# Performance work log

Hardware: AMD Instinct MI355X
Metric: run time of the kernel (lower is better)

The kernel has to match this reference:

```python
import jax, jax.numpy as jnp
import numpy as np
import math

B, L, D, H = 2, 2048, 1024, 16
HD = D // H  # head dim = 64


def setup_inputs() -> dict:
    key = jax.random.key(0)
    ks = jax.random.split(key, 5)
    s = 0.02
    return {
        "x": jax.random.normal(ks[0], (B, L, D), dtype=jnp.float32),
        "w_qkv": jax.random.normal(ks[1], (D, 3 * D), dtype=jnp.float32) * s,
        "b_qkv": jnp.zeros((3 * D,), dtype=jnp.float32),
        "w_out": jax.random.normal(ks[2], (D, D), dtype=jnp.float32) * s,
        "b_out": jnp.zeros((D,), dtype=jnp.float32),
    }


def reference(x, w_qkv, b_qkv, w_out, b_out):
    Bc, Lc, Dc = x.shape
    qkv = x @ w_qkv + b_qkv  # [B, L, 3D]
    q, k, v = jnp.split(qkv, 3, axis=-1)
    # [B, H, L, hd]
    q = q.reshape(Bc, Lc, H, HD).transpose(0, 2, 1, 3)
    k = k.reshape(Bc, Lc, H, HD).transpose(0, 2, 1, 3)
    v = v.reshape(Bc, Lc, H, HD).transpose(0, 2, 1, 3)
    scores = jnp.einsum("bhqd,bhkd->bhqk", q, k) / math.sqrt(HD)
    causal = jnp.tril(jnp.ones((Lc, Lc), dtype=bool))
    scores = jnp.where(causal[None, None, :, :], scores, -jnp.inf)
    probs = jax.nn.softmax(scores, axis=-1)
    outs = jnp.einsum("bhqk,bhkd->bhqd", probs, v)  # [B, H, L, hd]
    outs = outs.transpose(0, 2, 1, 3).reshape(Bc, Lc, Dc)
    return outs @ w_out + b_out
```

## Files before the change

### kernel.cpp

```cpp
#include <hip/hip_runtime.h>
#include <hip/hip_bf16.h>


using bf16x8 = __attribute__((ext_vector_type(8))) short;
using f32x4  = __attribute__((ext_vector_type(4))) float;

static __device__ __forceinline__ unsigned short f2b(float f) {
  unsigned u = __builtin_bit_cast(unsigned, f);
  unsigned r = (u + 0x7fffu + ((u >> 16) & 1u)) >> 16;
  return (unsigned short)r;
}

static __device__ __forceinline__ unsigned cvtpk(float lo, float hi) {
  unsigned r;
  asm("v_cvt_pk_bf16_f32 %0, %1, %2" : "=v"(r) : "v"(lo), "v"(hi));
  return r;
}

static __device__ __forceinline__ void gl_lds16(const void* g, void* l) {
  __builtin_amdgcn_global_load_lds(
      (const __attribute__((address_space(1))) unsigned int*)g,
      (__attribute__((address_space(3))) unsigned int*)l, 16, 0, 0);
}

__global__ __launch_bounds__(256) void prep_inputs(
    const float* __restrict__ x, const float* __restrict__ w_qkv,
    const float* __restrict__ w_out, unsigned short* __restrict__ xb,
    unsigned short* __restrict__ wqkvt, unsigned short* __restrict__ woutt) {
  const int bid = blockIdx.x, t = threadIdx.x;
  if (bid < 2048) {
    int i = bid * 256 + t;
    const float4* p = reinterpret_cast<const float4*>(x) + (size_t)i * 2;
    float4 a = p[0], b = p[1];
    bf16x8 o;
    o[0] = f2b(a.x); o[1] = f2b(a.y); o[2] = f2b(a.z); o[3] = f2b(a.w);
    o[4] = f2b(b.x); o[5] = f2b(b.y); o[6] = f2b(b.z); o[7] = f2b(b.w);
    reinterpret_cast<bf16x8*>(xb)[i] = o;
  } else if (bid < 3584) {
    int idx = (bid - 2048) * 256 + t;
    int n = idx % 3072, k0 = (idx / 3072) * 8;
    if (k0 < 1024) {
      bf16x8 o;
#pragma unroll
      for (int j = 0; j < 8; ++j) o[j] = f2b(w_qkv[(size_t)(k0 + j) * 3072 + n]);
      *reinterpret_cast<bf16x8*>(&wqkvt[(size_t)n * 1024 + k0]) = o;
    }
  } else {
    int idx = (bid - 3584) * 256 + t;
    int n = idx % 1024, k0 = (idx / 1024) * 8;
    if (k0 < 1024) {
      bf16x8 o;
#pragma unroll
      for (int j = 0; j < 8; ++j) o[j] = f2b(w_out[(size_t)(k0 + j) * 1024 + n]);
      *reinterpret_cast<bf16x8*>(&woutt[(size_t)n * 1024 + k0]) = o;
    }
  }
}

__global__ __launch_bounds__(256) void transpose_v(
    const unsigned short* __restrict__ vb, unsigned short* __restrict__ vt) {
  __shared__ unsigned short T[64][72];
  const int bh = blockIdx.y, l0 = blockIdx.x * 64;
  const int row = threadIdx.x >> 2;
  const int qc  = threadIdx.x & 3;
#pragma unroll
  for (int h = 0; h < 2; ++h) {
    bf16x8 v = *reinterpret_cast<const bf16x8*>(
        &vb[((size_t)bh * 2048 + l0 + row) * 64 + h * 32 + qc * 8]);
#pragma unroll
    for (int j = 0; j < 8; ++j) T[h * 32 + qc * 8 + j][row] = (unsigned short)v[j];
  }
  __syncthreads();
#pragma unroll
  for (int h = 0; h < 2; ++h) {
    bf16x8 o = *reinterpret_cast<const bf16x8*>(&T[row][h * 32 + qc * 8]);
    *reinterpret_cast<bf16x8*>(
        &vt[((size_t)bh * 64 + row) * 2048 + l0 + h * 32 + qc * 8]) = o;
  }
}

__global__ __launch_bounds__(512) void gemm_qkv(
    const unsigned short* __restrict__ A,
    const unsigned short* __restrict__ Bt,
    const float* __restrict__ bias,
    unsigned short* __restrict__ qb, unsigned short* __restrict__ kb,
    unsigned short* __restrict__ vb) {
  __shared__ __align__(16) unsigned short lA[256 * 64];
  __shared__ __align__(16) unsigned short lB[128 * 64];
  const int t = threadIdx.x;
  const int lin = blockIdx.y * 24 + blockIdx.x;
  const int nb  = (lin & 7) * 48 + (lin >> 3);
  const int bm = nb / 24, bn = nb % 24;
  const int s0 = (nb * 5) & 15;
  const int w = t >> 6, lane = t & 63;
  const int lr = lane & 15, lg = lane >> 4;
  const int wm = (w >> 1) * 64, wn = (w & 1) * 64;
  const int g8  = lane >> 3;
  const int swz = ((lane & 7) * 16) ^ (g8 << 4);

  f32x4 acc[4][4];
#pragma unroll
  for (int i = 0; i < 4; ++i)
#pragma unroll
    for (int j = 0; j < 4; ++j) acc[i][j] = f32x4{0.f, 0.f, 0.f, 0.f};

  const size_t am = (size_t)bm * 256, bnr = (size_t)bn * 128;

  for (int kt = 0; kt < 16; ++kt) {
    const int k0 = ((kt + s0) & 15) * 64;
#pragma unroll
    for (int i = 0; i < 4; ++i) {
      const int rs = i * 64 + w * 8;
      gl_lds16((const char*)(A + (am + rs + g8) * 1024 + k0) + swz,
               (char*)lA + rs * 128);
    }
#pragma unroll
    for (int i = 0; i < 2; ++i) {
      const int rs = i * 64 + w * 8;
      gl_lds16((const char*)(Bt + (bnr + rs + g8) * 1024 + k0) + swz,
               (char*)lB + rs * 128);
    }
    __syncthreads();
#pragma unroll
    for (int kk = 0; kk < 64; kk += 32) {
      bf16x8 af[4], bfr[4];
#pragma unroll
      for (int fm = 0; fm < 4; ++fm) {
        int row = wm + fm * 16 + lr;
        af[fm] = *reinterpret_cast<const bf16x8*>(
            (const char*)lA + row * 128 + ((2 * kk + lg * 16) ^ ((lr & 7) << 4)));
      }
#pragma unroll
      for (int fn = 0; fn < 4; ++fn) {
        int row = wn + fn * 16 + lr;
        bfr[fn] = *reinterpret_cast<const bf16x8*>(
            (const char*)lB + row * 128 + ((2 * kk + lg * 16) ^ ((lr & 7) << 4)));
      }
#pragma unroll
      for (int fm = 0; fm < 4; ++fm)
#pragma unroll
        for (int fn = 0; fn < 4; ++fn)
          acc[fm][fn] = __builtin_amdgcn_mfma_f32_16x16x32_bf16(
              af[fm], bfr[fn], acc[fm][fn], 0, 0, 0);
    }
    __syncthreads();
  }

#pragma unroll
  for (int fm = 0; fm < 4; ++fm) {
#pragma unroll
    for (int fn = 0; fn < 4; ++fn) {
#pragma unroll
      for (int r = 0; r < 4; ++r) {
        int row = bm * 256 + wm + fm * 16 + lg * 4 + r;
        int col = bn * 128 + wn + fn * 16 + lr;
        float v = acc[fm][fn][r] + bias[col];
        int bb = row >> 11, l = row & 2047;
        int which = col >> 10, hn = col & 1023;
        int h = hn >> 6, d = hn & 63;
        int bh = bb * 16 + h;
        if (which == 0)
          qb[((size_t)bh * 2048 + l) * 64 + d] = f2b(v * 0.180336879f);
        else if (which == 1)
          kb[((size_t)bh * 2048 + l) * 64 + d] = f2b(v);
        else
          vb[((size_t)bh * 2048 + l) * 64 + d] = f2b(v);
      }
    }
  }
}

__global__ __launch_bounds__(256) void gemm_out(
    const unsigned short* __restrict__ A,
    const unsigned short* __restrict__ Bt,
    const float* __restrict__ bias, float* __restrict__ outf) {
  __shared__ __align__(16) unsigned short lA[128 * 64];
  __shared__ __align__(16) unsigned short lB[64 * 64];
  const int t = threadIdx.x;
  const int lin = blockIdx.y * 16 + blockIdx.x;
  const int nb  = (lin & 7) * 64 + (lin >> 3);
  const int bm = nb >> 4, bn = nb & 15;
  const int s0 = (nb * 5) & 15;
  const int w = t >> 6, lane = t & 63;
  const int lr = lane & 15, lg = lane >> 4;
  const int wm = (w >> 1) * 64, wn = (w & 1) * 32;
  const int g8  = lane >> 3;
  const int swz = ((lane & 7) * 16) ^ (g8 << 4);

  f32x4 acc[4][2];
#pragma unroll
  for (int i = 0; i < 4; ++i)
#pragma unroll
    for (int j = 0; j < 2; ++j) acc[i][j] = f32x4{0.f, 0.f, 0.f, 0.f};

  const size_t am = (size_t)bm * 128, bnr = (size_t)bn * 64;

  for (int kt = 0; kt < 16; ++kt) {
    const int k0 = ((kt + s0) & 15) * 64;
#pragma unroll
    for (int i = 0; i < 4; ++i) {
      const int rs = i * 32 + w * 8;
      gl_lds16((const char*)(A + (am + rs + g8) * 1024 + k0) + swz,
               (char*)lA + rs * 128);
    }
#pragma unroll
    for (int i = 0; i < 2; ++i) {
      const int rs = i * 32 + w * 8;
      gl_lds16((const char*)(Bt + (bnr + rs + g8) * 1024 + k0) + swz,
               (char*)lB + rs * 128);
    }
    __syncthreads();
#pragma unroll
    for (int kk = 0; kk < 64; kk += 32) {
      bf16x8 af[4], bfr[2];
#pragma unroll
      for (int fm = 0; fm < 4; ++fm) {
        int row = wm + fm * 16 + lr;
        af[fm] = *reinterpret_cast<const bf16x8*>(
            (const char*)lA + row * 128 + ((2 * kk + lg * 16) ^ ((lr & 7) << 4)));
      }
#pragma unroll
      for (int fn = 0; fn < 2; ++fn) {
        int row = wn + fn * 16 + lr;
        bfr[fn] = *reinterpret_cast<const bf16x8*>(
            (const char*)lB + row * 128 + ((2 * kk + lg * 16) ^ ((lr & 7) << 4)));
      }
#pragma unroll
      for (int fm = 0; fm < 4; ++fm)
#pragma unroll
        for (int fn = 0; fn < 2; ++fn)
          acc[fm][fn] = __builtin_amdgcn_mfma_f32_16x16x32_bf16(
              af[fm], bfr[fn], acc[fm][fn], 0, 0, 0);
    }
    __syncthreads();
  }

#pragma unroll
  for (int fm = 0; fm < 4; ++fm)
#pragma unroll
    for (int fn = 0; fn < 2; ++fn)
#pragma unroll
      for (int r = 0; r < 4; ++r) {
        int row = bm * 128 + wm + fm * 16 + lg * 4 + r;
        int col = bn * 64 + wn + fn * 16 + lr;
        outf[(size_t)row * 1024 + col] = acc[fm][fn][r] + bias[col];
      }
}

__global__ __launch_bounds__(256, 2) void attn_kernel(
    const unsigned short* __restrict__ qb, const unsigned short* __restrict__ kb,
    const unsigned short* __restrict__ vt, unsigned short* __restrict__ attnb) {
  __shared__ __align__(16) unsigned short lK[2][128 * 64];
  __shared__ __align__(16) unsigned short lV[2][2][64 * 64];
  __shared__ __align__(16) unsigned short pl[4][16 * 128];
  const int bid = blockIdx.x;
  const int xcd = bid & 7, pos = bid >> 3;
  const int half = pos >> 5, idx = pos & 31;
  const int bh = xcd * 4 + half * 2 + (idx >> 4);
  const int qt = half ? (15 - (idx & 15)) : (idx & 15);
  const int q0 = qt * 128;
  const int w = threadIdx.x >> 6, lane = threadIdx.x & 63;
  const int lr = lane & 15, lg = lane >> 4;
  const int g8  = lane >> 3;
  const int swz = ((lane & 7) * 16) ^ (g8 << 4);

  const unsigned short* Kg = kb + (size_t)bh * 2048 * 64;
  const unsigned short* Vg = vt + (size_t)bh * 64 * 2048;

  auto stage = [&](int buf, int c) {
    const size_t kv0 = (size_t)c * 128;
#pragma unroll
    for (int i = 0; i < 4; ++i) {
      const int rs = i * 32 + w * 8;
      gl_lds16((const char*)(Kg + (kv0 + rs + g8) * 64) + swz,
               (char*)&lK[buf][0] + rs * 128);
    }
#pragma unroll
    for (int h = 0; h < 2; ++h)
#pragma unroll
      for (int i = 0; i < 2; ++i) {
        const int rs = i * 32 + w * 8;
        gl_lds16((const char*)(Vg + (size_t)(rs + g8) * 2048 + kv0 + h * 64) + swz,
                 (char*)&lV[buf][h][0] + rs * 128);
      }
  };

  bf16x8 qf[2][2];
#pragma unroll
  for (int qi = 0; qi < 2; ++qi)
#pragma unroll
    for (int kk = 0; kk < 2; ++kk)
      qf[qi][kk] = *reinterpret_cast<const bf16x8*>(
          &qb[((size_t)bh * 2048 + q0 + w * 32 + qi * 16 + lr) * 64 + kk * 32 + lg * 8]);

  f32x4 acc[2][4];
#pragma unroll
  for (int qi = 0; qi < 2; ++qi)
#pragma unroll
    for (int i = 0; i < 4; ++i) acc[qi][i] = f32x4{0.f, 0.f, 0.f, 0.f};
  float m[2] = {-1e30f, -1e30f}, rs[2] = {0.f, 0.f};

  const int nc = qt + 1;
  stage(0, 0);

  for (int c = 0; c < nc; ++c) {
    const int cur = c & 1;
    __syncthreads();
    if (c + 1 < nc) stage(cur ^ 1, c + 1);

    f32x4 s[2][8];
#pragma unroll
    for (int qi = 0; qi < 2; ++qi)
#pragma unroll
      for (int i = 0; i < 8; ++i) s[qi][i] = f32x4{0.f, 0.f, 0.f, 0.f};
    __builtin_amdgcn_s_setprio(1);
#pragma unroll
    for (int nf = 0; nf < 8; ++nf) {
      const int row = nf * 16 + lr;
      bf16x8 k0 = *reinterpret_cast<const bf16x8*>(
          (const char*)&lK[cur][0] + row * 128 + ((lg * 16) ^ ((lr & 7) << 4)));
      bf16x8 k1 = *reinterpret_cast<const bf16x8*>(
          (const char*)&lK[cur][0] + row * 128 + ((64 + lg * 16) ^ ((lr & 7) << 4)));
#pragma unroll
      for (int qi = 0; qi < 2; ++qi) {
        s[qi][nf] = __builtin_amdgcn_mfma_f32_16x16x32_bf16(k0, qf[qi][0], s[qi][nf], 0, 0, 0);
        s[qi][nf] = __builtin_amdgcn_mfma_f32_16x16x32_bf16(k1, qf[qi][1], s[qi][nf], 0, 0, 0);
      }
    }
    __builtin_amdgcn_s_setprio(0);

#pragma unroll
    for (int qi = 0; qi < 2; ++qi) {
      const int qrow = q0 + w * 32 + qi * 16 + lr;
      const bool diag = (c * 128 + 127) > (q0 + w * 32 + qi * 16);
      float ps[8][4];
      float mx = -1e30f;
      if (diag) {
#pragma unroll
        for (int nf = 0; nf < 8; ++nf)
#pragma unroll
          for (int r = 0; r < 4; ++r) {
            int key = c * 128 + nf * 16 + lg * 4 + r;
            float sv = (key <= qrow) ? s[qi][nf][r] : -1e30f;
            ps[nf][r] = sv;
            mx = fmaxf(mx, sv);
          }
      } else {
#pragma unroll
        for (int nf = 0; nf < 8; ++nf)
#pragma unroll
          for (int r = 0; r < 4; ++r) {
            ps[nf][r] = s[qi][nf][r];
            mx = fmaxf(mx, ps[nf][r]);
          }
      }
      mx = fmaxf(mx, __shfl_xor(mx, 16));
      mx = fmaxf(mx, __shfl_xor(mx, 32));
      if (__any(mx > m[qi] + 8.f)) {
        float mn = fmaxf(m[qi], mx);
        float scl = exp2f(m[qi] - mn);
        m[qi] = mn;
        rs[qi] *= scl;
#pragma unroll
        for (int df = 0; df < 4; ++df) acc[qi][df] *= scl;
      }
      float ss = 0.f;
#pragma unroll
      for (int nf = 0; nf < 8; ++nf)
#pragma unroll
        for (int r = 0; r < 4; ++r) {
          float pe = exp2f(ps[nf][r] - m[qi]);
          ps[nf][r] = pe;
          ss += pe;
        }
      ss += __shfl_xor(ss, 16);
      ss += __shfl_xor(ss, 32);
      rs[qi] += ss;

#pragma unroll
      for (int nf = 0; nf < 8; ++nf) {
        uint2 pk;
        pk.x = cvtpk(ps[nf][0], ps[nf][1]);
        pk.y = cvtpk(ps[nf][2], ps[nf][3]);
        *reinterpret_cast<uint2*>(
            (char*)&pl[w][0] + lr * 256 + ((nf * 32 + lg * 8) ^ ((lr & 7) << 4))) = pk;
      }
      __builtin_amdgcn_s_setprio(1);
#pragma unroll
      for (int kk = 0; kk < 4; ++kk) {
        bf16x8 pf = *reinterpret_cast<const bf16x8*>(
            (const char*)&pl[w][0] + lr * 256 + ((kk * 64 + lg * 16) ^ ((lr & 7) << 4)));
#pragma unroll
        for (int df = 0; df < 4; ++df) {
          const int row = df * 16 + lr;
          bf16x8 vf = *reinterpret_cast<const bf16x8*>(
              (const char*)&lV[cur][kk >> 1][0] + row * 128 +
              (((kk & 1) * 64 + lg * 16) ^ ((lr & 7) << 4)));
          acc[qi][df] = __builtin_amdgcn_mfma_f32_16x16x32_bf16(vf, pf, acc[qi][df], 0, 0, 0);
        }
      }
      __builtin_amdgcn_s_setprio(0);
    }
  }

  const int b = bh >> 4, h = bh & 15;
#pragma unroll
  for (int qi = 0; qi < 2; ++qi) {
    float inv = 1.f / rs[qi];
    int qrow = q0 + w * 32 + qi * 16 + lr;
#pragma unroll
    for (int df = 0; df < 4; ++df) {
      ushort4 ov;
      ov.x = f2b(acc[qi][df][0] * inv); ov.y = f2b(acc[qi][df][1] * inv);
      ov.z = f2b(acc[qi][df][2] * inv); ov.w = f2b(acc[qi][df][3] * inv);
      *reinterpret_cast<ushort4*>(
          &attnb[((size_t)b * 2048 + qrow) * 1024 + h * 64 + df * 16 + lg * 4]) = ov;
    }
  }
}

extern "C" void kernel_launch(void* const* d_in, const int* in_sizes, int n_in,
                              void* d_out, int out_size, void* d_ws, size_t ws_size,
                              hipStream_t stream) {
  const float* x     = (const float*)d_in[0];
  const float* w_qkv = (const float*)d_in[1];
  const float* b_qkv = (const float*)d_in[2];
  const float* w_out = (const float*)d_in[3];
  const float* b_out = (const float*)d_in[4];
  float* out = (float*)d_out;
  char* ws = (char*)d_ws;

  unsigned short* xb    = (unsigned short*)(ws);
  unsigned short* vt    = (unsigned short*)(ws);
  unsigned short* wqkvt = (unsigned short*)(ws + 8388608);
  unsigned short* woutt = (unsigned short*)(ws + 14680064);
  unsigned short* qb    = (unsigned short*)(ws + 16777216);
  unsigned short* kb    = (unsigned short*)(ws + 25165824);
  unsigned short* vb    = (unsigned short*)(ws + 33554432);
  unsigned short* attnb = (unsigned short*)(ws + 41943040);

  prep_inputs<<<4096, 256, 0, stream>>>(x, w_qkv, w_out, xb, wqkvt, woutt);
  gemm_qkv<<<dim3(24, 16), 512, 0, stream>>>(xb, wqkvt, b_qkv, qb, kb, vb);
  transpose_v<<<dim3(32, 32), 256, 0, stream>>>(vb, vt);
  attn_kernel<<<512, 256, 0, stream>>>(qb, kb, vt, attnb);
  gemm_out<<<dim3(16, 32), 256, 0, stream>>>(attnb, woutt, b_out, out);
}
```

Baseline: 129.6 us.

## Shrink attention tiles to 64 queries and 64 keys, doubling grid and occupancy

```diff
diff --git a/kernel.cpp b/kernel.cpp
--- a/kernel.cpp
+++ b/kernel.cpp
@@ -247,18 +247,19 @@
       }
 }
 
-__global__ __launch_bounds__(256, 2) void attn_kernel(
+__global__ __launch_bounds__(256, 4) void attn_kernel(
     const unsigned short* __restrict__ qb, const unsigned short* __restrict__ kb,
     const unsigned short* __restrict__ vt, unsigned short* __restrict__ attnb) {
-  __shared__ __align__(16) unsigned short lK[2][128 * 64];
-  __shared__ __align__(16) unsigned short lV[2][2][64 * 64];
-  __shared__ __align__(16) unsigned short pl[4][16 * 128];
+  __shared__ __align__(16) unsigned short lK[2][64 * 64];
+  __shared__ __align__(16) unsigned short lV[2][64 * 64];
+  __shared__ __align__(16) unsigned short pl[4][16 * 64];
   const int bid = blockIdx.x;
   const int xcd = bid & 7, pos = bid >> 3;
-  const int half = pos >> 5, idx = pos & 31;
-  const int bh = xcd * 4 + half * 2 + (idx >> 4);
-  const int qt = half ? (15 - (idx & 15)) : (idx & 15);
-  const int q0 = qt * 128;
+  const int half = pos >> 6, idx = pos & 63;
+  const int bh = xcd * 4 + half * 2 + (idx >> 5);
+  const int j = idx & 31;
+  const int qt = half ? (31 - j) : j;
+  const int q0 = qt * 64;
   const int w = threadIdx.x >> 6, lane = threadIdx.x & 63;
   const int lr = lane & 15, lg = lane >> 4;
   const int g8  = lane >> 3;
@@ -268,37 +269,32 @@
   const unsigned short* Vg = vt + (size_t)bh * 64 * 2048;
 
   auto stage = [&](int buf, int c) {
-    const size_t kv0 = (size_t)c * 128;
-#pragma unroll
-    for (int i = 0; i < 4; ++i) {
+    const size_t kv0 = (size_t)c * 64;
+#pragma unroll
+    for (int i = 0; i < 2; ++i) {
       const int rs = i * 32 + w * 8;
       gl_lds16((const char*)(Kg + (kv0 + rs + g8) * 64) + swz,
                (char*)&lK[buf][0] + rs * 128);
     }
 #pragma unroll
-    for (int h = 0; h < 2; ++h)
-#pragma unroll
-      for (int i = 0; i < 2; ++i) {
-        const int rs = i * 32 + w * 8;
-        gl_lds16((const char*)(Vg + (size_t)(rs + g8) * 2048 + kv0 + h * 64) + swz,
-                 (char*)&lV[buf][h][0] + rs * 128);
-      }
+    for (int i = 0; i < 2; ++i) {
+      const int rs = i * 32 + w * 8;
+      gl_lds16((const char*)(Vg + (size_t)(rs + g8) * 2048 + kv0) + swz,
+               (char*)&lV[buf][0] + rs * 128);
+    }
   };
 
-  bf16x8 qf[2][2];
-#pragma unroll
-  for (int qi = 0; qi < 2; ++qi)
-#pragma unroll
-    for (int kk = 0; kk < 2; ++kk)
-      qf[qi][kk] = *reinterpret_cast<const bf16x8*>(
-          &qb[((size_t)bh * 2048 + q0 + w * 32 + qi * 16 + lr) * 64 + kk * 32 + lg * 8]);
-
-  f32x4 acc[2][4];
-#pragma unroll
-  for (int qi = 0; qi < 2; ++qi)
-#pragma unroll
-    for (int i = 0; i < 4; ++i) acc[qi][i] = f32x4{0.f, 0.f, 0.f, 0.f};
-  float m[2] = {-1e30f, -1e30f}, rs[2] = {0.f, 0.f};
+  const int qrow = q0 + w * 16 + lr;
+  bf16x8 qf[2];
+#pragma unroll
+  for (int kk = 0; kk < 2; ++kk)
+    qf[kk] = *reinterpret_cast<const bf16x8*>(
+        &qb[((size_t)bh * 2048 + qrow) * 64 + kk * 32 + lg * 8]);
+
+  f32x4 acc[4];
+#pragma unroll
+  for (int i = 0; i < 4; ++i) acc[i] = f32x4{0.f, 0.f, 0.f, 0.f};
+  float m = -1e30f, rsum = 0.f;
 
   const int nc = qt + 1;
   stage(0, 0);
@@ -308,114 +304,97 @@
     __syncthreads();
     if (c + 1 < nc) stage(cur ^ 1, c + 1);
 
-    f32x4 s[2][8];
-#pragma unroll
-    for (int qi = 0; qi < 2; ++qi)
-#pragma unroll
-      for (int i = 0; i < 8; ++i) s[qi][i] = f32x4{0.f, 0.f, 0.f, 0.f};
-    __builtin_amdgcn_s_setprio(1);
-#pragma unroll
-    for (int nf = 0; nf < 8; ++nf) {
+    f32x4 s[4];
+#pragma unroll
+    for (int i = 0; i < 4; ++i) s[i] = f32x4{0.f, 0.f, 0.f, 0.f};
+#pragma unroll
+    for (int nf = 0; nf < 4; ++nf) {
       const int row = nf * 16 + lr;
       bf16x8 k0 = *reinterpret_cast<const bf16x8*>(
           (const char*)&lK[cur][0] + row * 128 + ((lg * 16) ^ ((lr & 7) << 4)));
       bf16x8 k1 = *reinterpret_cast<const bf16x8*>(
           (const char*)&lK[cur][0] + row * 128 + ((64 + lg * 16) ^ ((lr & 7) << 4)));
-#pragma unroll
-      for (int qi = 0; qi < 2; ++qi) {
-        s[qi][nf] = __builtin_amdgcn_mfma_f32_16x16x32_bf16(k0, qf[qi][0], s[qi][nf], 0, 0, 0);
-        s[qi][nf] = __builtin_amdgcn_mfma_f32_16x16x32_bf16(k1, qf[qi][1], s[qi][nf], 0, 0, 0);
-      }
-    }
-    __builtin_amdgcn_s_setprio(0);
-
-#pragma unroll
-    for (int qi = 0; qi < 2; ++qi) {
-      const int qrow = q0 + w * 32 + qi * 16 + lr;
-      const bool diag = (c * 128 + 127) > (q0 + w * 32 + qi * 16);
-      float ps[8][4];
-      float mx = -1e30f;
-      if (diag) {
-#pragma unroll
-        for (int nf = 0; nf < 8; ++nf)
-#pragma unroll
-          for (int r = 0; r < 4; ++r) {
-            int key = c * 128 + nf * 16 + lg * 4 + r;
-            float sv = (key <= qrow) ? s[qi][nf][r] : -1e30f;
-            ps[nf][r] = sv;
-            mx = fmaxf(mx, sv);
-          }
-      } else {
-#pragma unroll
-        for (int nf = 0; nf < 8; ++nf)
-#pragma unroll
-          for (int r = 0; r < 4; ++r) {
-            ps[nf][r] = s[qi][nf][r];
-            mx = fmaxf(mx, ps[nf][r]);
-          }
-      }
-      mx = fmaxf(mx, __shfl_xor(mx, 16));
-      mx = fmaxf(mx, __shfl_xor(mx, 32));
-      if (__any(mx > m[qi] + 8.f)) {
-        float mn = fmaxf(m[qi], mx);
-        float scl = exp2f(m[qi] - mn);
-        m[qi] = mn;
-        rs[qi] *= scl;
-#pragma unroll
-        for (int df = 0; df < 4; ++df) acc[qi][df] *= scl;
-      }
-      float ss = 0.f;
-#pragma unroll
-      for (int nf = 0; nf < 8; ++nf)
+      s[nf] = __builtin_amdgcn_mfma_f32_16x16x32_bf16(k0, qf[0], s[nf], 0, 0, 0);
+      s[nf] = __builtin_amdgcn_mfma_f32_16x16x32_bf16(k1, qf[1], s[nf], 0, 0, 0);
+    }
+
+    const bool diag = (c * 64 + 63) > (q0 + w * 16);
+    float ps[4][4];
+    float mx = -1e30f;
+    if (diag) {
+#pragma unroll
+      for (int nf = 0; nf < 4; ++nf)
 #pragma unroll
         for (int r = 0; r < 4; ++r) {
-          float pe = exp2f(ps[nf][r] - m[qi]);
-          ps[nf][r] = pe;
-          ss += pe;
+          int key = c * 64 + nf * 16 + lg * 4 + r;
+          float sv = (key <= qrow) ? s[nf][r] : -1e30f;
+          ps[nf][r] = sv;
+          mx = fmaxf(mx, sv);
         }
-      ss += __shfl_xor(ss, 16);
-      ss += __shfl_xor(ss, 32);
-      rs[qi] += ss;
-
-#pragma unroll
-      for (int nf = 0; nf < 8; ++nf) {
-        uint2 pk;
-        pk.x = cvtpk(ps[nf][0], ps[nf][1]);
-        pk.y = cvtpk(ps[nf][2], ps[nf][3]);
-        *reinterpret_cast<uint2*>(
-            (char*)&pl[w][0] + lr * 256 + ((nf * 32 + lg * 8) ^ ((lr & 7) << 4))) = pk;
-      }
-      __builtin_amdgcn_s_setprio(1);
-#pragma unroll
-      for (int kk = 0; kk < 4; ++kk) {
-        bf16x8 pf = *reinterpret_cast<const bf16x8*>(
-            (const char*)&pl[w][0] + lr * 256 + ((kk * 64 + lg * 16) ^ ((lr & 7) << 4)));
-#pragma unroll
-        for (int df = 0; df < 4; ++df) {
-          const int row = df * 16 + lr;
-          bf16x8 vf = *reinterpret_cast<const bf16x8*>(
-              (const char*)&lV[cur][kk >> 1][0] + row * 128 +
-              (((kk & 1) * 64 + lg * 16) ^ ((lr & 7) << 4)));
-          acc[qi][df] = __builtin_amdgcn_mfma_f32_16x16x32_bf16(vf, pf, acc[qi][df], 0, 0, 0);
+    } else {
+#pragma unroll
+      for (int nf = 0; nf < 4; ++nf)
+#pragma unroll
+        for (int r = 0; r < 4; ++r) {
+          ps[nf][r] = s[nf][r];
+          mx = fmaxf(mx, ps[nf][r]);
         }
-      }
-      __builtin_amdgcn_s_setprio(0);
+    }
+    mx = fmaxf(mx, __shfl_xor(mx, 16));
+    mx = fmaxf(mx, __shfl_xor(mx, 32));
+    if (__any(mx > m + 8.f)) {
+      float mn = fmaxf(m, mx);
+      float scl = exp2f(m - mn);
+      m = mn;
+      rsum *= scl;
+#pragma unroll
+      for (int df = 0; df < 4; ++df) acc[df] *= scl;
+    }
+    float ss = 0.f;
+#pragma unroll
+    for (int nf = 0; nf < 4; ++nf)
+#pragma unroll
+      for (int r = 0; r < 4; ++r) {
+        float pe = exp2f(ps[nf][r] - m);
+        ps[nf][r] = pe;
+        ss += pe;
+      }
+    ss += __shfl_xor(ss, 16);
+    ss += __shfl_xor(ss, 32);
+    rsum += ss;
+
+#pragma unroll
+    for (int nf = 0; nf < 4; ++nf) {
+      uint2 pk;
+      pk.x = cvtpk(ps[nf][0], ps[nf][1]);
+      pk.y = cvtpk(ps[nf][2], ps[nf][3]);
+      *reinterpret_cast<uint2*>(
+          (char*)&pl[w][0] + lr * 128 + ((nf * 32 + lg * 8) ^ ((lr & 7) << 4))) = pk;
+    }
+#pragma unroll
+    for (int kk = 0; kk < 2; ++kk) {
+      bf16x8 pf = *reinterpret_cast<const bf16x8*>(
+          (const char*)&pl[w][0] + lr * 128 + ((kk * 64 + lg * 16) ^ ((lr & 7) << 4)));
+#pragma unroll
+      for (int df = 0; df < 4; ++df) {
+        const int row = df * 16 + lr;
+        bf16x8 vf = *reinterpret_cast<const bf16x8*>(
+            (const char*)&lV[cur][0] + row * 128 +
+            ((kk * 64 + lg * 16) ^ ((lr & 7) << 4)));
+        acc[df] = __builtin_amdgcn_mfma_f32_16x16x32_bf16(vf, pf, acc[df], 0, 0, 0);
+      }
     }
   }
 
   const int b = bh >> 4, h = bh & 15;
-#pragma unroll
-  for (int qi = 0; qi < 2; ++qi) {
-    float inv = 1.f / rs[qi];
-    int qrow = q0 + w * 32 + qi * 16 + lr;
-#pragma unroll
-    for (int df = 0; df < 4; ++df) {
-      ushort4 ov;
-      ov.x = f2b(acc[qi][df][0] * inv); ov.y = f2b(acc[qi][df][1] * inv);
-      ov.z = f2b(acc[qi][df][2] * inv); ov.w = f2b(acc[qi][df][3] * inv);
-      *reinterpret_cast<ushort4*>(
-          &attnb[((size_t)b * 2048 + qrow) * 1024 + h * 64 + df * 16 + lg * 4]) = ov;
-    }
+  float inv = 1.f / rsum;
+#pragma unroll
+  for (int df = 0; df < 4; ++df) {
+    ushort4 ov;
+    ov.x = f2b(acc[df][0] * inv); ov.y = f2b(acc[df][1] * inv);
+    ov.z = f2b(acc[df][2] * inv); ov.w = f2b(acc[df][3] * inv);
+    *reinterpret_cast<ushort4*>(
+        &attnb[((size_t)b * 2048 + qrow) * 1024 + h * 64 + df * 16 + lg * 4]) = ov;
   }
 }
 
@@ -442,6 +421,6 @@
   prep_inputs<<<4096, 256, 0, stream>>>(x, w_qkv, w_out, xb, wqkvt, woutt);
   gemm_qkv<<<dim3(24, 16), 512, 0, stream>>>(xb, wqkvt, b_qkv, qb, kb, vb);
   transpose_v<<<dim3(32, 32), 256, 0, stream>>>(vb, vt);
-  attn_kernel<<<512, 256, 0, stream>>>(qb, kb, vt, attnb);
+  attn_kernel<<<1024, 256, 0, stream>>>(qb, kb, vt, attnb);
   gemm_out<<<dim3(16, 32), 256, 0, stream>>>(attnb, woutt, b_out, out);
 }
```

After: 121.7 us. 1.07x faster.
